# Performance work log

Hardware: AMD Instinct MI355X
Metric: run time of the kernel (lower is better)

Reference implementation:

```python
import jax, jax.numpy as jnp
import numpy as np

C = 256
EPS = 1e-5

def setup_inputs() -> dict:
    key = jax.random.key(0)
    ks = jax.random.split(key, 10)
    N, H, W = 4, 64, 64
    Ch = C // 2
    sc = 1.0 / np.sqrt(C)
    sch = 1.0 / np.sqrt(Ch)
    return {
        "x": jax.random.normal(ks[0], (N, C, H, W), dtype=jnp.float32),
        "cfc": jax.random.normal(ks[1], (C, 2), dtype=jnp.float32) * 0.1,
        "theta_w": jax.random.normal(ks[2], (Ch, C), dtype=jnp.float32) * sc,
        "theta_b": jax.random.normal(ks[3], (Ch,), dtype=jnp.float32) * 0.01,
        "phi_w": jax.random.normal(ks[4], (Ch, C), dtype=jnp.float32) * sc,
        "phi_b": jax.random.normal(ks[5], (Ch,), dtype=jnp.float32) * 0.01,
        "g_w": jax.random.normal(ks[6], (Ch, C), dtype=jnp.float32) * sc,
        "g_b": jax.random.normal(ks[7], (Ch,), dtype=jnp.float32) * 0.01,
        "out_w": jax.random.normal(ks[8], (C, Ch), dtype=jnp.float32) * sch,
        "out_b": jax.random.normal(ks[9], (C,), dtype=jnp.float32) * 0.01,
    }

def reference(x, cfc, theta_w, theta_b, phi_w, phi_b, g_w, g_b, out_w, out_b):
    N, Cc, H, W = x.shape
    L = H * W
    xf = x.reshape(N, Cc, L)
    # SRM style pooling: per-channel mean and (unbiased) std over spatial dims
    mean = jnp.mean(xf, axis=2)                              # [N,C]
    var = jnp.var(xf, axis=2, ddof=1) + EPS                  # torch .var() is unbiased
    std = jnp.sqrt(var)
    # style integration: z = mean*cfc[:,0] + std*cfc[:,1], gate = sigmoid(z)
    z = mean * cfc[None, :, 0] + std * cfc[None, :, 1]       # [N,C]
    gate = jax.nn.sigmoid(z)[:, :, None]                     # [N,C,1]
    s = xf * gate                                            # srm_out flattened [N,C,L]
    # 1x1 convs == per-pixel linear maps
    theta = jnp.einsum('oc,ncl->nol', theta_w, s) + theta_b[None, :, None]  # [N,C/2,L]
    phi = jnp.einsum('oc,ncl->nol', phi_w, s) + phi_b[None, :, None]
    g = jnp.einsum('oc,ncl->nol', g_w, s) + g_b[None, :, None]
    # attention[n,i,j] = sum_c theta[n,c,i]*phi[n,c,j]; softmax over j (no 1/sqrt(d))
    attn = jax.nn.softmax(jnp.einsum('nci,ncj->nij', theta, phi), axis=-1)  # [N,L,L]
    # nl_out[n,c,i] = sum_j g[n,c,j]*attn[n,i,j]
    nl = jnp.einsum('ncj,nij->nci', g, attn)                 # [N,C/2,L]
    nl = jnp.einsum('oc,ncl->nol', out_w, nl) + out_b[None, :, None]        # [N,C,L]
    out = s + nl
    return out.reshape(N, Cc, H, W)
```

## Files before the change

### kernel.cpp

```cpp
#include <hip/hip_runtime.h>
#include <hip/hip_bf16.h>

#define LSP 4096
#define NC  256
#define NH  128
#define KB  64
#define QW  32
#define SPLIT 4
#define NTILE ((LSP / SPLIT) / KB)

typedef __attribute__((ext_vector_type(8))) short short8;
typedef __attribute__((ext_vector_type(4))) float f32x4;
typedef __attribute__((ext_vector_type(4))) unsigned int u32x4;
typedef __attribute__((ext_vector_type(2))) unsigned int u32x2;
typedef __hip_bfloat16 bf16;

#define MFMA16(a,b,c) __builtin_amdgcn_mfma_f32_16x16x32_bf16((a),(b),(c),0,0,0)

typedef __attribute__((address_space(1))) const void gas_t;
typedef __attribute__((address_space(3))) void las_t;
#define GLDS16(g, l) __builtin_amdgcn_global_load_lds((gas_t*)(g), (las_t*)(l), 16, 0, 0)

static __device__ __forceinline__ unsigned short f2bf(float f) {
  bf16 h = __float2bfloat16(f);
  return __builtin_bit_cast(unsigned short, h);
}
static __device__ __forceinline__ unsigned int packbf2(float a, float b) {
  return (unsigned int)f2bf(a) | ((unsigned int)f2bf(b) << 16);
}
static __device__ __forceinline__ float bf2f(unsigned short u) {
  return __builtin_bit_cast(float, (unsigned int)u << 16);
}
static __device__ __forceinline__ unsigned short bfu(bf16 h) {
  return __builtin_bit_cast(unsigned short, h);
}

__global__ __launch_bounds__(256) void k_pre(const float* __restrict__ a0,
    const float* __restrict__ a1, const float* __restrict__ a2,
    const float* __restrict__ a3, const float* __restrict__ tb,
    const float* __restrict__ pb, bf16* __restrict__ dst, float* __restrict__ bcat,
    const float* __restrict__ x, const float* __restrict__ cfc,
    float* __restrict__ gate) {
  int b = blockIdx.x;
  if (b < 512) {
    int i = b * 256 + threadIdx.x;
    int seg = i >> 15, off = i & 32767;
    const float* s = (seg == 0) ? a0 : (seg == 1) ? a1 : (seg == 2) ? a2 : a3;
    dst[i] = __float2bfloat16(s[off]);
    if (b == 0)
      bcat[threadIdx.x] = threadIdx.x < 128 ? tb[threadIdx.x] : pb[threadIdx.x - 128];
    return;
  }
  int nc = b - 512;
  const float4* x4 = (const float4*)(x + (size_t)nc * LSP);
  float s = 0.f, q = 0.f;
  for (int i = threadIdx.x; i < LSP / 4; i += 256) {
    float4 v = x4[i];
    s += v.x + v.y + v.z + v.w;
    q += v.x * v.x + v.y * v.y + v.z * v.z + v.w * v.w;
  }
#pragma unroll
  for (int o = 32; o > 0; o >>= 1) { s += __shfl_xor(s, o); q += __shfl_xor(q, o); }
  __shared__ float rs[4], rq[4];
  int w = threadIdx.x >> 6;
  if ((threadIdx.x & 63) == 0) { rs[w] = s; rq[w] = q; }
  __syncthreads();
  if (threadIdx.x == 0) {
    float S = rs[0] + rs[1] + rs[2] + rs[3];
    float Q = rq[0] + rq[1] + rq[2] + rq[3];
    float mean = S / (float)LSP;
    float var = (Q - S * S / (float)LSP) / (float)(LSP - 1) + 1e-5f;
    float sd = sqrtf(var);
    int c = nc & (NC - 1);
    float z = mean * cfc[2 * c] + sd * cfc[2 * c + 1];
    gate[nc] = 1.f / (1.f + __expf(-z));
  }
}

__global__ __launch_bounds__(256) void k_scale_t(const float* __restrict__ x,
    const float* __restrict__ gate, bf16* __restrict__ s_t) {
  __shared__ bf16 T[64][66];
  int n = blockIdx.z;
  int c0 = blockIdx.y * 64;
  int l0 = blockIdx.x * 64;
  int tid = threadIdx.x;
  int lr = tid & 63, cr = tid >> 6;
#pragma unroll
  for (int k = 0; k < 16; ++k) {
    int c = cr * 16 + k;
    float gv = gate[n * NC + c0 + c];
    float v = x[((size_t)(n * NC + c0 + c)) * LSP + l0 + lr] * gv;
    T[c][lr] = __float2bfloat16(v);
  }
  __syncthreads();
  int cg = tid & 7, lw = tid >> 3;
#pragma unroll
  for (int ps = 0; ps < 2; ++ps) {
    int l = lw + ps * 32;
    unsigned int pk[4];
#pragma unroll
    for (int e = 0; e < 4; ++e)
      pk[e] = (unsigned int)bfu(T[cg * 8 + 2 * e][l]) |
              ((unsigned int)bfu(T[cg * 8 + 2 * e + 1][l]) << 16);
    *(u32x4*)(s_t + ((size_t)n * LSP + l0 + l) * NC + c0 + cg * 8) =
        *(const u32x4*)pk;
  }
}

static __device__ __forceinline__ void gemm_nt_body(const bf16* __restrict__ A,
    const bf16* __restrict__ B, const float* __restrict__ bias, int bias_row,
    bf16* __restrict__ D, int Nd, int Kd, int bx) {
  int tn = Nd >> 6;
  int m0 = (bx / tn) * 64, n0 = (bx % tn) * 64;
  int tid = threadIdx.x, w = tid >> 6, lane = tid & 63;
  int lo = lane & 15, g = lane >> 4;
  f32x4 zero = {0.f, 0.f, 0.f, 0.f};
  f32x4 acc[4];
#pragma unroll
  for (int i = 0; i < 4; ++i) acc[i] = zero;
  for (int kc = 0; kc < Kd; kc += 32) {
    short8 bfr = *(const short8*)(B + (size_t)(n0 + w * 16 + lo) * Kd + kc + g * 8);
#pragma unroll
    for (int i = 0; i < 4; ++i) {
      short8 afr = *(const short8*)(A + (size_t)(m0 + 16 * i + lo) * Kd + kc + g * 8);
      acc[i] = MFMA16(afr, bfr, acc[i]);
    }
  }
  int col = n0 + w * 16 + lo;
#pragma unroll
  for (int i = 0; i < 4; ++i)
#pragma unroll
    for (int r = 0; r < 4; ++r) {
      int row = m0 + 16 * i + g * 4 + r;
      float bv = bias_row ? bias[row] : bias[col];
      D[(size_t)row * Nd + col] = __float2bfloat16(acc[i][r] + bv);
    }
}

__global__ __launch_bounds__(256) void k_gemms(const bf16* __restrict__ s_t,
    const bf16* __restrict__ wbf, const float* __restrict__ bcat,
    const float* __restrict__ g_b, bf16* __restrict__ thph, bf16* __restrict__ gTb) {
  int z = blockIdx.z, bx = blockIdx.x;
  if (bx < 256) {
    gemm_nt_body(s_t + (size_t)z * LSP * NC, wbf, bcat, 0,
                 thph + (size_t)z * LSP * 256, 256, NC, bx);
  } else {
    gemm_nt_body(wbf + 65536, s_t + (size_t)z * LSP * NC, g_b, 1,
                 gTb + (size_t)z * NH * LSP, LSP, NC, bx - 256);
  }
}

__global__ __launch_bounds__(512, 2) void k_attn(const bf16* __restrict__ thph,
    const bf16* __restrict__ gT, bf16* __restrict__ Opart, float* __restrict__ ml) {
  __shared__ bf16 Kl[3][KB * NH];
  __shared__ bf16 Vl[3][NH * KB];
  __shared__ bf16 Pl[8][QW * KB];

  const int n = blockIdx.z, sp = blockIdx.y;
  const int tid = threadIdx.x, w = tid >> 6, lane = tid & 63;
  const int lo = lane & 15, g = lane >> 4;
  const int swz = (lo & 7) << 4;

  const bf16* thn = thph + (size_t)n * LSP * 256;
  const bf16* gv  = gT + (size_t)n * NH * LSP;
  const int q0 = blockIdx.x * 256 + w * QW;
  const int j0base = sp * (LSP / SPLIT);

  short8 qf[2][4];
#pragma unroll
  for (int qs = 0; qs < 2; ++qs)
#pragma unroll
    for (int kc = 0; kc < 4; ++kc)
      qf[qs][kc] = *(const short8*)(thn + (size_t)(q0 + qs * 16 + lo) * 256 + kc * 32 + g * 8);

  size_t koff[2], voff[2];
  int ldso[2];
#pragma unroll
  for (int i = 0; i < 2; ++i) {
    int ci = i * 512 + tid;
    int kj = ci >> 4, kcc = ci & 15;
    koff[i] = (size_t)kj * 256 + 128 + ((kcc ^ (kj & 7)) * 8);
    int vd = ci >> 3, vc2 = ci & 7;
    voff[i] = (size_t)vd * LSP + ((vc2 ^ (vd & 7)) * 8);
    ldso[i] = ci * 16;
  }

#define STAGE(JT, BUF) do { \
    const bf16* ksrc = thn + (size_t)(j0base + (JT) * KB) * 256; \
    const bf16* vsrc = gv + (j0base + (JT) * KB); \
    char* kdst = (char*)&Kl[BUF][0]; \
    char* vdst = (char*)&Vl[BUF][0]; \
    _Pragma("unroll") \
    for (int i = 0; i < 2; ++i) { \
      GLDS16(ksrc + koff[i], kdst + ldso[i]); \
      GLDS16(vsrc + voff[i], vdst + ldso[i]); \
    } } while (0)

  f32x4 zero = {0.f, 0.f, 0.f, 0.f};
  f32x4 acc[2][8];
#pragma unroll
  for (int qs = 0; qs < 2; ++qs)
#pragma unroll
    for (int dc = 0; dc < 8; ++dc) acc[qs][dc] = zero;
  float mv[2] = {-1e30f, -1e30f};
  float ls[2] = {0.f, 0.f};

  STAGE(0, 0);
  STAGE(1, 1);

  char* pwb = (char*)&Pl[w][0];

  for (int t = 0; t < NTILE; ++t) {
    int cur = t % 3;
    if (t < NTILE - 1) asm volatile("s_waitcnt vmcnt(4)" ::: "memory");
    else               asm volatile("s_waitcnt vmcnt(0)" ::: "memory");
    __builtin_amdgcn_sched_barrier(0);
    __builtin_amdgcn_s_barrier();
    __builtin_amdgcn_sched_barrier(0);
    if (t + 2 < NTILE) STAGE(t + 2, (t + 2) % 3);

    const char* Kb = (const char*)&Kl[cur][0];
    const char* Vb = (const char*)&Vl[cur][0];

    short8 kfr[4][4];
#pragma unroll
    for (int jt = 0; jt < 4; ++jt)
#pragma unroll
      for (int kc = 0; kc < 4; ++kc)
        kfr[jt][kc] = *(const short8*)(Kb + (jt * 16 + lo) * 256 + ((kc * 64 + g * 16) ^ swz));

    f32x4 st[2][4];
#pragma unroll
    for (int qs = 0; qs < 2; ++qs)
#pragma unroll
      for (int jt = 0; jt < 4; ++jt) st[qs][jt] = zero;
    __builtin_amdgcn_s_setprio(1);
#pragma unroll
    for (int kc = 0; kc < 4; ++kc)
#pragma unroll
      for (int jt = 0; jt < 4; ++jt) {
        st[0][jt] = MFMA16(kfr[jt][kc], qf[0][kc], st[0][jt]);
        st[1][jt] = MFMA16(kfr[jt][kc], qf[1][kc], st[1][jt]);
      }
    __builtin_amdgcn_s_setprio(0);

#pragma unroll
    for (int qs = 0; qs < 2; ++qs) {
      float t0 = fmaxf(fmaxf(st[qs][0][0], st[qs][0][1]), fmaxf(st[qs][0][2], st[qs][0][3]));
      float t1 = fmaxf(fmaxf(st[qs][1][0], st[qs][1][1]), fmaxf(st[qs][1][2], st[qs][1][3]));
      float t2 = fmaxf(fmaxf(st[qs][2][0], st[qs][2][1]), fmaxf(st[qs][2][2], st[qs][2][3]));
      float t3 = fmaxf(fmaxf(st[qs][3][0], st[qs][3][1]), fmaxf(st[qs][3][2], st[qs][3][3]));
      float tq = fmaxf(fmaxf(t0, t1), fmaxf(t2, t3));
      tq = fmaxf(tq, __shfl_xor(tq, 16));
      tq = fmaxf(tq, __shfl_xor(tq, 32));

      if (__any(tq > mv[qs] + 8.f)) {
        float nm = fmaxf(mv[qs], tq);
        float a = __expf(mv[qs] - nm);
        mv[qs] = nm; ls[qs] *= a;
#pragma unroll
        for (int r = 0; r < 4; ++r) {
          float b = __shfl(a, g * 4 + r);
#pragma unroll
          for (int dc = 0; dc < 8; ++dc) acc[qs][dc][r] *= b;
        }
      }

      float mm = mv[qs], psum = 0.f;
      int rowb = (qs * 16 + lo) * 128;
#pragma unroll
      for (int jt = 0; jt < 4; ++jt) {
        float e0 = __expf(st[qs][jt][0] - mm);
        float e1 = __expf(st[qs][jt][1] - mm);
        float e2 = __expf(st[qs][jt][2] - mm);
        float e3 = __expf(st[qs][jt][3] - mm);
        psum += (e0 + e1) + (e2 + e3);
        u32x2 pk;
        pk.x = packbf2(e0, e1);
        pk.y = packbf2(e2, e3);
        *(u32x2*)(pwb + rowb + ((jt * 32 + g * 8) ^ swz)) = pk;
      }
      psum += __shfl_xor(psum, 16);
      psum += __shfl_xor(psum, 32);
      ls[qs] += psum;
    }

    asm volatile("" ::: "memory");
#pragma unroll
    for (int kc2 = 0; kc2 < 2; ++kc2) {
      int kbb = kc2 * 64 + g * 16;
      short8 pa0 = *(const short8*)(pwb + lo * 128 + (kbb ^ swz));
      short8 pa1 = *(const short8*)(pwb + (16 + lo) * 128 + (kbb ^ swz));
      __builtin_amdgcn_s_setprio(1);
#pragma unroll
      for (int dc = 0; dc < 8; ++dc) {
        int d = dc * 16 + lo;
        short8 vb = *(const short8*)(Vb + d * 128 + (kbb ^ ((d & 7) << 4)));
        acc[0][dc] = MFMA16(pa0, vb, acc[0][dc]);
        acc[1][dc] = MFMA16(pa1, vb, acc[1][dc]);
      }
      __builtin_amdgcn_s_setprio(0);
    }
  }

  bf16* opb = Opart + ((size_t)(sp * 4 + n) * LSP + q0) * NH;
#pragma unroll
  for (int qs = 0; qs < 2; ++qs)
#pragma unroll
    for (int dc = 0; dc < 8; ++dc)
#pragma unroll
      for (int r = 0; r < 4; ++r)
        opb[(size_t)(qs * 16 + g * 4 + r) * NH + dc * 16 + lo] =
            __float2bfloat16(acc[qs][dc][r]);
  if (g == 0) {
    float2* mlp = (float2*)ml + (size_t)(sp * 4 + n) * LSP + q0;
#pragma unroll
    for (int qs = 0; qs < 2; ++qs)
      mlp[qs * 16 + lo] = make_float2(mv[qs], ls[qs]);
  }
#undef STAGE
}

__global__ __launch_bounds__(256) void k_final(const bf16* __restrict__ Wo,
    const bf16* __restrict__ Opart, const float* __restrict__ ml,
    const float* __restrict__ x, const float* __restrict__ gate,
    const float* __restrict__ ob, float* __restrict__ out) {
  int n = blockIdx.z;
  int m0 = (blockIdx.x >> 6) * 64, n0 = (blockIdx.x & 63) * 64;
  int tid = threadIdx.x, w = tid >> 6, lane = tid & 63;
  int lo = lane & 15, g = lane >> 4;
  int col = n0 + w * 16 + lo;

  float sc[SPLIT];
  {
    float2 m4[SPLIT];
    float mx = -1e30f;
#pragma unroll
    for (int s = 0; s < SPLIT; ++s) {
      m4[s] = ((const float2*)ml)[(size_t)(s * 4 + n) * LSP + col];
      mx = fmaxf(mx, m4[s].x);
    }
    float den = 0.f;
#pragma unroll
    for (int s = 0; s < SPLIT; ++s) { sc[s] = __expf(m4[s].x - mx); den += m4[s].y * sc[s]; }
    float inv = 1.f / den;
#pragma unroll
    for (int s = 0; s < SPLIT; ++s) sc[s] *= inv;
  }

  f32x4 zero = {0.f, 0.f, 0.f, 0.f};
  f32x4 acc[4];
#pragma unroll
  for (int i = 0; i < 4; ++i) acc[i] = zero;
#pragma unroll
  for (int kc = 0; kc < 4; ++kc) {
    float bv[8] = {0.f, 0.f, 0.f, 0.f, 0.f, 0.f, 0.f, 0.f};
#pragma unroll
    for (int s = 0; s < SPLIT; ++s) {
      short8 v = *(const short8*)(Opart + ((size_t)(s * 4 + n) * LSP + col) * NH + kc * 32 + g * 8);
#pragma unroll
      for (int e = 0; e < 8; ++e)
        bv[e] += sc[s] * bf2f((unsigned short)v[e]);
    }
    u32x4 pk4;
    pk4.x = packbf2(bv[0], bv[1]); pk4.y = packbf2(bv[2], bv[3]);
    pk4.z = packbf2(bv[4], bv[5]); pk4.w = packbf2(bv[6], bv[7]);
    short8 bfr = __builtin_bit_cast(short8, pk4);
#pragma unroll
    for (int i = 0; i < 4; ++i) {
      short8 afr = *(const short8*)(Wo + (size_t)(m0 + 16 * i + lo) * NH + kc * 32 + g * 8);
      acc[i] = MFMA16(afr, bfr, acc[i]);
    }
  }
#pragma unroll
  for (int i = 0; i < 4; ++i)
#pragma unroll
    for (int r = 0; r < 4; ++r) {
      int c = m0 + 16 * i + g * 4 + r;
      size_t xo = ((size_t)(n * NC + c)) * LSP + col;
      out[xo] = acc[i][r] + ob[c] + x[xo] * gate[n * NC + c];
    }
}

extern "C" void kernel_launch(void* const* d_in, const int* in_sizes, int n_in,
                              void* d_out, int out_size, void* d_ws, size_t ws_size,
                              hipStream_t stream) {
  const float* x       = (const float*)d_in[0];
  const float* cfc     = (const float*)d_in[1];
  const float* theta_w = (const float*)d_in[2];
  const float* theta_b = (const float*)d_in[3];
  const float* phi_w   = (const float*)d_in[4];
  const float* phi_b   = (const float*)d_in[5];
  const float* g_w     = (const float*)d_in[6];
  const float* g_b     = (const float*)d_in[7];
  const float* out_w   = (const float*)d_in[8];
  const float* out_b   = (const float*)d_in[9];
  float* out = (float*)d_out;

  char* p = (char*)d_ws;
  auto alloc = [&](size_t bytes) { char* r = p; p += (bytes + 255) & ~(size_t)255; return r; };
  float* gate  = (float*)alloc(4 * NC * sizeof(float));
  bf16* s_t    = (bf16*)alloc((size_t)4 * LSP * NC * 2);
  bf16* thph   = (bf16*)alloc((size_t)4 * LSP * 256 * 2);
  bf16* gTb    = (bf16*)alloc((size_t)4 * NH * LSP * 2);
  bf16* wbf    = (bf16*)alloc((size_t)4 * 32768 * 2);
  float* bcat  = (float*)alloc(256 * sizeof(float));
  bf16* Opart  = (bf16*)alloc((size_t)SPLIT * 4 * LSP * NH * 2);
  float* ml    = (float*)alloc((size_t)SPLIT * 4 * LSP * 2 * 4);

  k_pre<<<1536, 256, 0, stream>>>(theta_w, phi_w, g_w, out_w, theta_b, phi_b,
                                  wbf, bcat, x, cfc, gate);
  k_scale_t<<<dim3(64, 4, 4), 256, 0, stream>>>(x, gate, s_t);
  k_gemms<<<dim3(384, 1, 4), 256, 0, stream>>>(s_t, wbf, bcat, g_b, thph, gTb);
  k_attn<<<dim3(LSP / 256, SPLIT, 4), 512, 0, stream>>>(thph, gTb, Opart, ml);
  k_final<<<dim3(256, 1, 4), 256, 0, stream>>>(wbf + 98304, Opart, ml, x, gate, out_b, out);
}
```

Measured before the change: 197.4 us.

## Shrink attention tiles, double the KV split, and restructure final combine via LDS

The attention kernel now uses 32-key tiles, 256-thread blocks of 128 queries, an 8-way split over keys and double buffering in place of triple buffering. The goal is more blocks and higher occupancy with less LDS per block. The final kernel is rewritten so each block first merges the split partials for 64 positions into LDS once, then runs a full 256x64 output GEMM. This removes the earlier repeated re-reading of partials for every channel tile. In exchange the attention loop takes more barrier-synchronised iterations with less prefetch depth, and the larger split doubles partial-output traffic.

```diff
diff --git a/kernel.cpp b/kernel.cpp
--- a/kernel.cpp
+++ b/kernel.cpp
@@ -4,9 +4,9 @@
 #define LSP 4096
 #define NC  256
 #define NH  128
-#define KB  64
+#define KB  32
 #define QW  32
-#define SPLIT 4
+#define SPLIT 8
 #define NTILE ((LSP / SPLIT) / KB)
 
 typedef __attribute__((ext_vector_type(8))) short short8;
@@ -150,20 +150,20 @@
   }
 }
 
-__global__ __launch_bounds__(512, 2) void k_attn(const bf16* __restrict__ thph,
+__global__ __launch_bounds__(256, 4) void k_attn(const bf16* __restrict__ thph,
     const bf16* __restrict__ gT, bf16* __restrict__ Opart, float* __restrict__ ml) {
-  __shared__ bf16 Kl[3][KB * NH];
-  __shared__ bf16 Vl[3][NH * KB];
-  __shared__ bf16 Pl[8][QW * KB];
+  __shared__ bf16 Kl[2][KB * NH];
+  __shared__ bf16 Vl[2][NH * KB];
+  __shared__ bf16 Pl[4][QW * KB];
 
   const int n = blockIdx.z, sp = blockIdx.y;
   const int tid = threadIdx.x, w = tid >> 6, lane = tid & 63;
   const int lo = lane & 15, g = lane >> 4;
-  const int swz = (lo & 7) << 4;
+  const int swzK = (lo & 7) << 4;
 
   const bf16* thn = thph + (size_t)n * LSP * 256;
   const bf16* gv  = gT + (size_t)n * NH * LSP;
-  const int q0 = blockIdx.x * 256 + w * QW;
+  const int q0 = blockIdx.x * 128 + w * QW;
   const int j0base = sp * (LSP / SPLIT);
 
   short8 qf[2][4];
@@ -173,15 +173,14 @@
     for (int kc = 0; kc < 4; ++kc)
       qf[qs][kc] = *(const short8*)(thn + (size_t)(q0 + qs * 16 + lo) * 256 + kc * 32 + g * 8);
 
-  size_t koff[2], voff[2];
-  int ldso[2];
+  int koff[2], voff[2], ldso[2];
 #pragma unroll
   for (int i = 0; i < 2; ++i) {
-    int ci = i * 512 + tid;
+    int ci = i * 256 + tid;
     int kj = ci >> 4, kcc = ci & 15;
-    koff[i] = (size_t)kj * 256 + 128 + ((kcc ^ (kj & 7)) * 8);
-    int vd = ci >> 3, vc2 = ci & 7;
-    voff[i] = (size_t)vd * LSP + ((vc2 ^ (vd & 7)) * 8);
+    koff[i] = kj * 256 + 128 + ((kcc ^ (kj & 7)) * 8);
+    int vd = ci >> 2, vc2 = ci & 3;
+    voff[i] = vd * LSP + ((vc2 ^ (vd & 3)) * 8);
     ldso[i] = ci * 16;
   }
 
@@ -206,41 +205,33 @@
   float ls[2] = {0.f, 0.f};
 
   STAGE(0, 0);
-  STAGE(1, 1);
 
   char* pwb = (char*)&Pl[w][0];
 
   for (int t = 0; t < NTILE; ++t) {
-    int cur = t % 3;
-    if (t < NTILE - 1) asm volatile("s_waitcnt vmcnt(4)" ::: "memory");
-    else               asm volatile("s_waitcnt vmcnt(0)" ::: "memory");
+    int cur = t & 1;
+    asm volatile("s_waitcnt vmcnt(0)" ::: "memory");
     __builtin_amdgcn_sched_barrier(0);
     __builtin_amdgcn_s_barrier();
     __builtin_amdgcn_sched_barrier(0);
-    if (t + 2 < NTILE) STAGE(t + 2, (t + 2) % 3);
+    if (t + 1 < NTILE) STAGE(t + 1, cur ^ 1);
 
     const char* Kb = (const char*)&Kl[cur][0];
     const char* Vb = (const char*)&Vl[cur][0];
 
-    short8 kfr[4][4];
-#pragma unroll
-    for (int jt = 0; jt < 4; ++jt)
-#pragma unroll
-      for (int kc = 0; kc < 4; ++kc)
-        kfr[jt][kc] = *(const short8*)(Kb + (jt * 16 + lo) * 256 + ((kc * 64 + g * 16) ^ swz));
-
-    f32x4 st[2][4];
+    f32x4 st[2][2];
 #pragma unroll
     for (int qs = 0; qs < 2; ++qs)
 #pragma unroll
-      for (int jt = 0; jt < 4; ++jt) st[qs][jt] = zero;
+      for (int jt = 0; jt < 2; ++jt) st[qs][jt] = zero;
     __builtin_amdgcn_s_setprio(1);
 #pragma unroll
     for (int kc = 0; kc < 4; ++kc)
 #pragma unroll
-      for (int jt = 0; jt < 4; ++jt) {
-        st[0][jt] = MFMA16(kfr[jt][kc], qf[0][kc], st[0][jt]);
-        st[1][jt] = MFMA16(kfr[jt][kc], qf[1][kc], st[1][jt]);
+      for (int jt = 0; jt < 2; ++jt) {
+        short8 ka = *(const short8*)(Kb + (jt * 16 + lo) * 256 + ((kc * 64 + g * 16) ^ swzK));
+        st[0][jt] = MFMA16(ka, qf[0][kc], st[0][jt]);
+        st[1][jt] = MFMA16(ka, qf[1][kc], st[1][jt]);
       }
     __builtin_amdgcn_s_setprio(0);
 
@@ -248,9 +239,7 @@
     for (int qs = 0; qs < 2; ++qs) {
       float t0 = fmaxf(fmaxf(st[qs][0][0], st[qs][0][1]), fmaxf(st[qs][0][2], st[qs][0][3]));
       float t1 = fmaxf(fmaxf(st[qs][1][0], st[qs][1][1]), fmaxf(st[qs][1][2], st[qs][1][3]));
-      float t2 = fmaxf(fmaxf(st[qs][2][0], st[qs][2][1]), fmaxf(st[qs][2][2], st[qs][2][3]));
-      float t3 = fmaxf(fmaxf(st[qs][3][0], st[qs][3][1]), fmaxf(st[qs][3][2], st[qs][3][3]));
-      float tq = fmaxf(fmaxf(t0, t1), fmaxf(t2, t3));
+      float tq = fmaxf(t0, t1);
       tq = fmaxf(tq, __shfl_xor(tq, 16));
       tq = fmaxf(tq, __shfl_xor(tq, 32));
 
@@ -267,9 +256,10 @@
       }
 
       float mm = mv[qs], psum = 0.f;
-      int rowb = (qs * 16 + lo) * 128;
-#pragma unroll
-      for (int jt = 0; jt < 4; ++jt) {
+      int rowb = (qs * 16 + lo) * 64;
+      int swzP = (lo & 3) << 4;
+#pragma unroll
+      for (int jt = 0; jt < 2; ++jt) {
         float e0 = __expf(st[qs][jt][0] - mm);
         float e1 = __expf(st[qs][jt][1] - mm);
         float e2 = __expf(st[qs][jt][2] - mm);
@@ -278,7 +268,7 @@
         u32x2 pk;
         pk.x = packbf2(e0, e1);
         pk.y = packbf2(e2, e3);
-        *(u32x2*)(pwb + rowb + ((jt * 32 + g * 8) ^ swz)) = pk;
+        *(u32x2*)(pwb + rowb + ((jt * 32 + g * 8) ^ swzP)) = pk;
       }
       psum += __shfl_xor(psum, 16);
       psum += __shfl_xor(psum, 32);
@@ -286,21 +276,17 @@
     }
 
     asm volatile("" ::: "memory");
-#pragma unroll
-    for (int kc2 = 0; kc2 < 2; ++kc2) {
-      int kbb = kc2 * 64 + g * 16;
-      short8 pa0 = *(const short8*)(pwb + lo * 128 + (kbb ^ swz));
-      short8 pa1 = *(const short8*)(pwb + (16 + lo) * 128 + (kbb ^ swz));
-      __builtin_amdgcn_s_setprio(1);
-#pragma unroll
-      for (int dc = 0; dc < 8; ++dc) {
-        int d = dc * 16 + lo;
-        short8 vb = *(const short8*)(Vb + d * 128 + (kbb ^ ((d & 7) << 4)));
-        acc[0][dc] = MFMA16(pa0, vb, acc[0][dc]);
-        acc[1][dc] = MFMA16(pa1, vb, acc[1][dc]);
-      }
-      __builtin_amdgcn_s_setprio(0);
-    }
+    short8 pa0 = *(const short8*)(pwb + lo * 64 + ((g * 16) ^ ((lo & 3) << 4)));
+    short8 pa1 = *(const short8*)(pwb + (16 + lo) * 64 + ((g * 16) ^ ((lo & 3) << 4)));
+    __builtin_amdgcn_s_setprio(1);
+#pragma unroll
+    for (int dc = 0; dc < 8; ++dc) {
+      int d = dc * 16 + lo;
+      short8 vb = *(const short8*)(Vb + d * 64 + ((g * 16) ^ ((d & 3) << 4)));
+      acc[0][dc] = MFMA16(pa0, vb, acc[0][dc]);
+      acc[1][dc] = MFMA16(pa1, vb, acc[1][dc]);
+    }
+    __builtin_amdgcn_s_setprio(0);
   }
 
   bf16* opb = Opart + ((size_t)(sp * 4 + n) * LSP + q0) * NH;
@@ -325,19 +311,19 @@
     const bf16* __restrict__ Opart, const float* __restrict__ ml,
     const float* __restrict__ x, const float* __restrict__ gate,
     const float* __restrict__ ob, float* __restrict__ out) {
+  __shared__ bf16 Ol[64 * NH];
   int n = blockIdx.z;
-  int m0 = (blockIdx.x >> 6) * 64, n0 = (blockIdx.x & 63) * 64;
-  int tid = threadIdx.x, w = tid >> 6, lane = tid & 63;
-  int lo = lane & 15, g = lane >> 4;
-  int col = n0 + w * 16 + lo;
-
-  float sc[SPLIT];
+  int l0 = blockIdx.x * 64;
+  int tid = threadIdx.x;
+
   {
+    int l = tid >> 2, q4 = tid & 3;
+    float sc[SPLIT];
     float2 m4[SPLIT];
     float mx = -1e30f;
 #pragma unroll
     for (int s = 0; s < SPLIT; ++s) {
-      m4[s] = ((const float2*)ml)[(size_t)(s * 4 + n) * LSP + col];
+      m4[s] = ((const float2*)ml)[(size_t)(s * 4 + n) * LSP + l0 + l];
       mx = fmaxf(mx, m4[s].x);
     }
     float den = 0.f;
@@ -346,39 +332,61 @@
     float inv = 1.f / den;
 #pragma unroll
     for (int s = 0; s < SPLIT; ++s) sc[s] *= inv;
-  }
-
+#pragma unroll
+    for (int k = 0; k < 4; ++k) {
+      int oct = q4 + 4 * k;
+      float o8[8] = {0.f, 0.f, 0.f, 0.f, 0.f, 0.f, 0.f, 0.f};
+#pragma unroll
+      for (int s = 0; s < SPLIT; ++s) {
+        short8 v = *(const short8*)(Opart + ((size_t)(s * 4 + n) * LSP + l0 + l) * NH + oct * 8);
+#pragma unroll
+        for (int e = 0; e < 8; ++e) o8[e] += sc[s] * bf2f((unsigned short)v[e]);
+      }
+      u32x4 pk4;
+      pk4.x = packbf2(o8[0], o8[1]); pk4.y = packbf2(o8[2], o8[3]);
+      pk4.z = packbf2(o8[4], o8[5]); pk4.w = packbf2(o8[6], o8[7]);
+      *(u32x4*)((char*)Ol + l * 256 + ((oct * 16) ^ ((l & 7) << 4))) = pk4;
+    }
+  }
+  __syncthreads();
+
+  int w = tid >> 6, lane = tid & 63;
+  int lo = lane & 15, g = lane >> 4;
   f32x4 zero = {0.f, 0.f, 0.f, 0.f};
-  f32x4 acc[4];
-#pragma unroll
-  for (int i = 0; i < 4; ++i) acc[i] = zero;
+  f32x4 acc[4][4];
+#pragma unroll
+  for (int i = 0; i < 4; ++i)
+#pragma unroll
+    for (int j = 0; j < 4; ++j) acc[i][j] = zero;
 #pragma unroll
   for (int kc = 0; kc < 4; ++kc) {
-    float bv[8] = {0.f, 0.f, 0.f, 0.f, 0.f, 0.f, 0.f, 0.f};
-#pragma unroll
-    for (int s = 0; s < SPLIT; ++s) {
-      short8 v = *(const short8*)(Opart + ((size_t)(s * 4 + n) * LSP + col) * NH + kc * 32 + g * 8);
-#pragma unroll
-      for (int e = 0; e < 8; ++e)
-        bv[e] += sc[s] * bf2f((unsigned short)v[e]);
-    }
-    u32x4 pk4;
-    pk4.x = packbf2(bv[0], bv[1]); pk4.y = packbf2(bv[2], bv[3]);
-    pk4.z = packbf2(bv[4], bv[5]); pk4.w = packbf2(bv[6], bv[7]);
-    short8 bfr = __builtin_bit_cast(short8, pk4);
+    short8 bfr[4];
+#pragma unroll
+    for (int lt = 0; lt < 4; ++lt) {
+      int l = lt * 16 + lo;
+      bfr[lt] = *(const short8*)((const char*)Ol + l * 256 + ((kc * 64 + g * 16) ^ ((l & 7) << 4)));
+    }
 #pragma unroll
     for (int i = 0; i < 4; ++i) {
-      short8 afr = *(const short8*)(Wo + (size_t)(m0 + 16 * i + lo) * NH + kc * 32 + g * 8);
-      acc[i] = MFMA16(afr, bfr, acc[i]);
+      short8 afr = *(const short8*)(Wo + (size_t)(w * 64 + 16 * i + lo) * NH + kc * 32 + g * 8);
+#pragma unroll
+      for (int lt = 0; lt < 4; ++lt)
+        acc[i][lt] = MFMA16(afr, bfr[lt], acc[i][lt]);
     }
   }
 #pragma unroll
   for (int i = 0; i < 4; ++i)
 #pragma unroll
     for (int r = 0; r < 4; ++r) {
-      int c = m0 + 16 * i + g * 4 + r;
-      size_t xo = ((size_t)(n * NC + c)) * LSP + col;
-      out[xo] = acc[i][r] + ob[c] + x[xo] * gate[n * NC + c];
+      int c = w * 64 + 16 * i + g * 4 + r;
+      float obc = ob[c];
+      float gc = gate[n * NC + c];
+#pragma unroll
+      for (int lt = 0; lt < 4; ++lt) {
+        int l = l0 + lt * 16 + lo;
+        size_t xo = ((size_t)(n * NC + c)) * LSP + l;
+        out[xo] = acc[i][lt][r] + obc + x[xo] * gc;
+      }
     }
 }
 
@@ -412,6 +420,6 @@
                                   wbf, bcat, x, cfc, gate);
   k_scale_t<<<dim3(64, 4, 4), 256, 0, stream>>>(x, gate, s_t);
   k_gemms<<<dim3(384, 1, 4), 256, 0, stream>>>(s_t, wbf, bcat, g_b, thph, gTb);
-  k_attn<<<dim3(LSP / 256, SPLIT, 4), 512, 0, stream>>>(thph, gTb, Opart, ml);
-  k_final<<<dim3(256, 1, 4), 256, 0, stream>>>(wbf + 98304, Opart, ml, x, gate, out_b, out);
-}
+  k_attn<<<dim3(LSP / 128, SPLIT, 4), 256, 0, stream>>>(thph, gTb, Opart, ml);
+  k_final<<<dim3(64, 1, 4), 256, 0, stream>>>(wbf + 98304, Opart, ml, x, gate, out_b, out);
+}
```

After: 234.6 us. 18.9% more time.
